# Performance work log

Hardware: AMD Instinct MI355X
Metric: run time of the kernel (lower is better)

Reference implementation:

```python
import jax, jax.numpy as jnp
import numpy as np

# Static routing config (must match init_kwargs)
E = 16          # num_experts
G = 4           # n_group
EPG = E // G    # experts per group
K = 4           # moe_router_topk
TOPK_GROUP = 2  # moe_topk_group
PER_GROUP_K = K // TOPK_GROUP


def setup_inputs() -> dict:
    key = jax.random.key(0)
    ks = jax.random.split(key, 9)
    B, T, C, H, HS = 2, 1024, 1024, 256, 2048
    std = 0.02
    return {
        'x': jax.random.normal(ks[0], (B, T, C), jnp.float32),
        'router_w': jax.random.normal(ks[1], (E, C), jnp.float32) * std,
        'correction_bias': jnp.zeros((E,), jnp.float32),
        'gate_w': jax.random.normal(ks[2], (E, C, H), jnp.float32) * std,
        'up_w': jax.random.normal(ks[3], (E, C, H), jnp.float32) * std,
        'down_w': jax.random.normal(ks[4], (E, H, C), jnp.float32) * std,
        'shared_gate_w': jax.random.normal(ks[5], (HS, C), jnp.float32) * std,
        'shared_up_w': jax.random.normal(ks[6], (HS, C), jnp.float32) * std,
        'shared_down_w': jax.random.normal(ks[7], (C, HS), jnp.float32) * std,
    }


def _route(xf, router_w, correction_bias):
    # Grouped sigmoid top-k routing (group_limited_greedy) with score correction bias.
    S = xf.shape[0]
    logits = xf @ router_w.T                       # [S, E]
    scores = jax.nn.sigmoid(logits)
    sb = scores + correction_bias                  # biased scores (selection only)
    # group score = sum of top (K // topk_group) biased scores within each group
    grp_top = jax.lax.top_k(sb.reshape(S, G, EPG), PER_GROUP_K)[0]
    group_scores = grp_top.sum(axis=-1)            # [S, G]
    _, group_idx = jax.lax.top_k(group_scores, TOPK_GROUP)
    group_mask = jnp.zeros((S, G), sb.dtype).at[jnp.arange(S)[:, None], group_idx].set(1.0)
    score_mask = jnp.broadcast_to(group_mask[:, :, None], (S, G, EPG)).reshape(S, E)
    masked = jnp.where(score_mask > 0, sb, -jnp.inf)
    _, topk_idx = jax.lax.top_k(masked, K)         # [S, K]
    # final weights come from UNBIASED sigmoid scores, renormalized over top-k
    w = jnp.take_along_axis(scores, topk_idx, axis=1)
    w = w / (w.sum(axis=-1, keepdims=True) + 1e-20)
    return topk_idx, w, scores


def reference(x, router_w, correction_bias, gate_w, up_w, down_w,
              shared_gate_w, shared_up_w, shared_down_w):
    B, T, C = x.shape
    S = B * T
    xf = x.reshape(S, C)
    # shared expert (always-on SwiGLU FFN)
    sg = xf @ shared_gate_w.T
    su = xf @ shared_up_w.T
    shared_out = (jax.nn.silu(sg) * su) @ shared_down_w.T          # [S, C]
    # routing
    topk_idx, w, _scores = _route(xf, router_w, correction_bias)
    combine = jnp.zeros((S, E), xf.dtype).at[jnp.arange(S)[:, None], topk_idx].add(w)  # [S, E]
    # routed experts: SwiGLU per expert (dense dispatch, combine weights fold the sparsity)
    g = jnp.einsum('sc,ech->esh', xf, gate_w)
    u = jnp.einsum('sc,ech->esh', xf, up_w)
    h = jax.nn.silu(g) * u                                         # [E, S, H]
    hw = h * combine.T[:, :, None]                                 # weight before down-proj
    routed = jnp.einsum('esh,ehc->sc', hw, down_w)                 # [S, C]
    return (shared_out + routed).reshape(B, T, C)
```

## Files before the change

### kernel.cpp

```cpp
#include <hip/hip_runtime.h>
#include <hip/hip_bf16.h>
#include <math.h>

#define S 2048
#define CDIM 1024
#define H 256
#define HS 2048
#define E 16
#define GNUM 4
#define EPG 4
#define TOPK 4
#define KSLICES 8

typedef __attribute__((ext_vector_type(8))) short bfrag_t;
typedef __attribute__((ext_vector_type(4))) float facc_t;
typedef __attribute__((ext_vector_type(4))) unsigned int u32x4;
typedef __attribute__((ext_vector_type(4))) unsigned short u16x4;

__device__ __forceinline__ float sigmoidf_(float v) { return 1.f / (1.f + __expf(-v)); }

__device__ __forceinline__ unsigned short f2bf(float f) {
    union { float f; unsigned u; } v; v.f = f;
    unsigned r = v.u + 0x7FFFu + ((v.u >> 16) & 1u);
    return (unsigned short)(r >> 16);
}
__device__ __forceinline__ float bf2f(unsigned short u) {
    union { unsigned u; float f; } v; v.u = ((unsigned)u) << 16; return v.f;
}
__device__ __forceinline__ unsigned long long pack4(float4 v) {
    return (unsigned long long)f2bf(v.x)
         | ((unsigned long long)f2bf(v.y) << 16)
         | ((unsigned long long)f2bf(v.z) << 32)
         | ((unsigned long long)f2bf(v.w) << 48);
}

__device__ __forceinline__ void stage16(const unsigned short* g, unsigned short* l, int lane) {
#if __has_builtin(__builtin_amdgcn_global_load_lds)
    __builtin_amdgcn_global_load_lds(
        (const __attribute__((address_space(1))) void*)g,
        (__attribute__((address_space(3))) void*)l, 16, 0, 0);
#else
    *(u32x4*)(l + lane * 8) = *(const u32x4*)g;
#endif
}

struct CastArgs {
    const float4* src[3];
    unsigned long long* dst[3];
};

#define LG_BLOCKS   ((S / 16) * KSLICES)
#define CAST_BLOCKS (3 * (HS * CDIM / 4 / 256))
#define TGU_BLOCKS  (2 * E * (CDIM / 64) * (H / 64))
#define TDN_BLOCKS  (E * (H / 64) * (CDIM / 64))

__global__ __launch_bounds__(256) void preproc_kernel(
    const float* __restrict__ x, const float* __restrict__ rw,
    float* __restrict__ lgpart, unsigned short* __restrict__ xb,
    CastArgs ca,
    const float* __restrict__ gate_w, unsigned short* __restrict__ gwT,
    const float* __restrict__ up_w,  unsigned short* __restrict__ uwT,
    const float* __restrict__ down_w, unsigned short* __restrict__ dwT)
{
    __shared__ __align__(16) float tbuf[64 * 65];
    const int tid = threadIdx.x;
    int id = blockIdx.x;

    if (id < LG_BLOCKS) {
        const int ks = id >> 7;
        const int s0 = (id & 127) * 16;
        const int t = tid & 15, e = tid >> 4;
        const float4* xp = (const float4*)(x + (size_t)(s0 + t) * CDIM + ks * (CDIM / KSLICES));
        const float4* wp = (const float4*)(rw + (size_t)e * CDIM + ks * (CDIM / KSLICES));
        float acc = 0.f;
#pragma unroll 8
        for (int c = 0; c < CDIM / KSLICES / 4; ++c) {
            float4 xv = xp[c], wv = wp[c];
            acc += xv.x * wv.x + xv.y * wv.y + xv.z * wv.z + xv.w * wv.w;
        }
        float4 v0 = xp[e * 2], v1 = xp[e * 2 + 1];
        unsigned long long* dst = (unsigned long long*)
            (xb + (size_t)(s0 + t) * CDIM + ks * (CDIM / KSLICES) + e * 8);
        dst[0] = pack4(v0);
        dst[1] = pack4(v1);
        lgpart[((size_t)ks * S + s0 + t) * E + e] = acc;
        return;
    }
    id -= LG_BLOCKS;

    if (id < CAST_BLOCKS) {
        const int buf = id >> 11;
        const int i = (id & 2047) * 256 + tid;
        ca.dst[buf][i] = pack4(ca.src[buf][i]);
        return;
    }
    id -= CAST_BLOCKS;

    const float* src; unsigned short* dst; int R, Cc, zz, c0, r0;
    if (id < TGU_BLOCKS) {
        const int bx = id & 3; const int by = (id >> 2) & 15; const int bz = id >> 6;
        R = CDIM; Cc = H;
        src = (bz < E) ? gate_w : up_w;
        dst = (bz < E) ? gwT : uwT;
        zz = (bz < E) ? bz : bz - E;
        c0 = bx * 64; r0 = by * 64;
    } else {
        id -= TGU_BLOCKS;
        const int bx = id & 15; const int by = (id >> 4) & 3; const int bz = id >> 6;
        R = H; Cc = CDIM;
        src = down_w; dst = dwT; zz = bz;
        c0 = bx * 64; r0 = by * 64;
    }
    const size_t mo = (size_t)zz * R * Cc;
    src += mo; dst += mo;
    const int tx = tid & 15, ty = tid >> 4;
#pragma unroll
    for (int i = 0; i < 4; ++i) {
        const int row = ty + 16 * i;
        float4 v = *(const float4*)&src[(size_t)(r0 + row) * Cc + c0 + tx * 4];
        float* p = &tbuf[row * 65 + tx * 4];
        p[0] = v.x; p[1] = v.y; p[2] = v.z; p[3] = v.w;
    }
    __syncthreads();
#pragma unroll
    for (int j = 0; j < 4; ++j) {
        const int c = ty + 16 * j;
        u16x4 o;
#pragma unroll
        for (int i = 0; i < 4; ++i)
            o[i] = f2bf(tbuf[(tx * 4 + i) * 65 + c]);
        *(u16x4*)&dst[(size_t)(c0 + c) * R + r0 + tx * 4] = o;
    }
}

__global__ __launch_bounds__(256) void route_kernel(
    const float* __restrict__ lgpart, const float* __restrict__ bias,
    int* __restrict__ counts, int* __restrict__ list, float* __restrict__ wlist)
{
    __shared__ int lcount[E];
    __shared__ int lbase[E];
    const int tid = threadIdx.x;
    const int s = blockIdx.x * 256 + tid;
    if (tid < E) lcount[tid] = 0;
    float lgv[E];
#pragma unroll
    for (int i = 0; i < E; ++i) lgv[i] = 0.f;
#pragma unroll
    for (int ks = 0; ks < KSLICES; ++ks) {
        const float4* p = (const float4*)(lgpart + ((size_t)ks * S + s) * E);
#pragma unroll
        for (int q = 0; q < 4; ++q) {
            float4 v = p[q];
            lgv[q * 4 + 0] += v.x; lgv[q * 4 + 1] += v.y;
            lgv[q * 4 + 2] += v.z; lgv[q * 4 + 3] += v.w;
        }
    }
    float sc[E], sb[E];
#pragma unroll
    for (int e2 = 0; e2 < E; ++e2) {
        sc[e2] = 1.f / (1.f + __expf(-lgv[e2]));
        sb[e2] = sc[e2] + bias[e2];
    }
    float gsc[GNUM];
#pragma unroll
    for (int g = 0; g < GNUM; ++g) {
        int b_ = g * EPG;
        int m1 = 0; float v1 = sb[b_];
#pragma unroll
        for (int j = 1; j < EPG; ++j) if (sb[b_ + j] > v1) { v1 = sb[b_ + j]; m1 = j; }
        float v2 = -1e30f;
#pragma unroll
        for (int j = 0; j < EPG; ++j) if (j != m1 && sb[b_ + j] > v2) v2 = sb[b_ + j];
        gsc[g] = v1 + v2;
    }
    int g1 = 0;
#pragma unroll
    for (int g = 1; g < GNUM; ++g) if (gsc[g] > gsc[g1]) g1 = g;
    int g2 = (g1 == 0) ? 1 : 0;
#pragma unroll
    for (int g = 0; g < GNUM; ++g) if (g != g1 && gsc[g] > gsc[g2]) g2 = g;
    bool allowed[E];
#pragma unroll
    for (int e2 = 0; e2 < E; ++e2) {
        int g = e2 >> 2;
        allowed[e2] = (g == g1) || (g == g2);
    }
    int idx[TOPK]; float wk[TOPK];
#pragma unroll
    for (int k = 0; k < TOPK; ++k) {
        int best = 0; float bv = -1e30f;
#pragma unroll
        for (int e2 = 0; e2 < E; ++e2)
            if (allowed[e2] && sb[e2] > bv) { bv = sb[e2]; best = e2; }
        allowed[best] = false;
        idx[k] = best;
        wk[k] = sc[best];
    }
    float inv = 1.f / (wk[0] + wk[1] + wk[2] + wk[3] + 1e-20f);
    __syncthreads();
    int lpos[TOPK];
#pragma unroll
    for (int k = 0; k < TOPK; ++k)
        lpos[k] = atomicAdd(&lcount[idx[k]], 1);
    __syncthreads();
    if (tid < E)
        lbase[tid] = atomicAdd(&counts[tid], lcount[tid]);
    __syncthreads();
#pragma unroll
    for (int k = 0; k < TOPK; ++k) {
        int ee = idx[k];
        int pos = lbase[ee] + lpos[k];
        list[ee * S + pos] = s | (k << 16);
        wlist[ee * S + pos] = wk[k] * inv;
    }
}


__global__ __launch_bounds__(256) void gemm_shared_gateup(
    const unsigned short* __restrict__ xb, const unsigned short* __restrict__ gb,
    const unsigned short* __restrict__ ub, unsigned short* __restrict__ shb)
{
    __shared__ __align__(16) unsigned short As[2 * 128 * 32];
    __shared__ __align__(16) unsigned short Bg[2 * 64 * 32];
    __shared__ __align__(16) unsigned short Bu[2 * 64 * 32];
    const int tid = threadIdx.x;
    const int lane = tid & 63, w = tid >> 6;
    const int l15 = lane & 15, q = lane >> 4;
    const int r0 = blockIdx.y * 128;
    const int c0 = blockIdx.x * 64;
    const int wr = (w >> 1) * 64, wc = (w & 1) * 32;
    const int Lrow = lane >> 2;
    const int gseg = (lane & 3) ^ ((lane >> 3) & 3);
    const unsigned short* gA1 = xb + (size_t)(r0 + w * 16 + Lrow) * CDIM + gseg * 8;
    const unsigned short* gA2 = gA1 + (size_t)64 * CDIM;
    const unsigned short* gG  = gb + (size_t)(c0 + w * 16 + Lrow) * CDIM + gseg * 8;
    const unsigned short* gU  = ub + (size_t)(c0 + w * 16 + Lrow) * CDIM + gseg * 8;
    unsigned short* lA1 = &As[(w * 16) * 32];
    unsigned short* lA2 = lA1 + 64 * 32;
    unsigned short* lG  = &Bg[(w * 16) * 32];
    unsigned short* lU  = &Bu[(w * 16) * 32];
    const int swq = (q ^ ((l15 >> 1) & 3)) * 8;
    facc_t accg[4][2], accu[4][2];
#pragma unroll
    for (int i = 0; i < 4; ++i)
#pragma unroll
        for (int j = 0; j < 2; ++j) { accg[i][j] = 0.f; accu[i][j] = 0.f; }
    for (int k0 = 0; k0 < CDIM; k0 += 64) {
        stage16(gA1 + k0,      lA1,             lane);
        stage16(gA1 + k0 + 32, lA1 + 128 * 32,  lane);
        stage16(gA2 + k0,      lA2,             lane);
        stage16(gA2 + k0 + 32, lA2 + 128 * 32,  lane);
        stage16(gG + k0,       lG,              lane);
        stage16(gG + k0 + 32,  lG + 64 * 32,    lane);
        stage16(gU + k0,       lU,              lane);
        stage16(gU + k0 + 32,  lU + 64 * 32,    lane);
        __syncthreads();
#pragma unroll
        for (int kk = 0; kk < 2; ++kk) {
            const unsigned short* Ah = &As[kk * 128 * 32];
            const unsigned short* Gh = &Bg[kk * 64 * 32];
            const unsigned short* Uh = &Bu[kk * 64 * 32];
            bfrag_t af[4], gf[2], uf[2];
#pragma unroll
            for (int i = 0; i < 4; ++i)
                af[i] = *(const bfrag_t*)&Ah[(wr + i * 16 + l15) * 32 + swq];
#pragma unroll
            for (int j = 0; j < 2; ++j) {
                gf[j] = *(const bfrag_t*)&Gh[(wc + j * 16 + l15) * 32 + swq];
                uf[j] = *(const bfrag_t*)&Uh[(wc + j * 16 + l15) * 32 + swq];
            }
#pragma unroll
            for (int i = 0; i < 4; ++i)
#pragma unroll
                for (int j = 0; j < 2; ++j) {
                    accg[i][j] = __builtin_amdgcn_mfma_f32_16x16x32_bf16(af[i], gf[j], accg[i][j], 0, 0, 0);
                    accu[i][j] = __builtin_amdgcn_mfma_f32_16x16x32_bf16(af[i], uf[j], accu[i][j], 0, 0, 0);
                }
        }
        __syncthreads();
    }
#pragma unroll
    for (int i = 0; i < 4; ++i)
#pragma unroll
        for (int j = 0; j < 2; ++j)
#pragma unroll
            for (int r = 0; r < 4; ++r) {
                int row = r0 + wr + i * 16 + q * 4 + r;
                int col = c0 + wc + j * 16 + l15;
                float g = accg[i][j][r], u = accu[i][j][r];
                shb[(size_t)row * HS + col] = f2bf(g * sigmoidf_(g) * u);
            }
}

__global__ __launch_bounds__(256) void gemm_shared_down(
    const unsigned short* __restrict__ shb, const unsigned short* __restrict__ db,
    const unsigned short* __restrict__ dbuf, float* __restrict__ out)
{
    __shared__ __align__(16) unsigned short As[2 * 64 * 32];
    __shared__ __align__(16) unsigned short Bs[2 * 64 * 32];
    const int tid = threadIdx.x;
    const int lane = tid & 63, w = tid >> 6;
    const int l15 = lane & 15, q = lane >> 4;
    const int r0 = blockIdx.y * 64;
    const int c0 = blockIdx.x * 64;
    const int wr = (w >> 1) * 32, wc = (w & 1) * 32;
    const int Lrow = lane >> 2;
    const int gseg = (lane & 3) ^ ((lane >> 3) & 3);
    const unsigned short* gA = shb + (size_t)(r0 + w * 16 + Lrow) * HS + gseg * 8;
    const unsigned short* gB = db + (size_t)(c0 + w * 16 + Lrow) * HS + gseg * 8;
    unsigned short* lA = &As[(w * 16) * 32];
    unsigned short* lB = &Bs[(w * 16) * 32];
    const int swq = (q ^ ((l15 >> 1) & 3)) * 8;
    facc_t acc[2][2];
#pragma unroll
    for (int i = 0; i < 2; ++i)
#pragma unroll
        for (int j = 0; j < 2; ++j) acc[i][j] = 0.f;
    for (int k0 = 0; k0 < HS; k0 += 64) {
        stage16(gA + k0,      lA,            lane);
        stage16(gA + k0 + 32, lA + 64 * 32,  lane);
        stage16(gB + k0,      lB,            lane);
        stage16(gB + k0 + 32, lB + 64 * 32,  lane);
        __syncthreads();
#pragma unroll
        for (int kk = 0; kk < 2; ++kk) {
            const unsigned short* Ah = &As[kk * 64 * 32];
            const unsigned short* Bh = &Bs[kk * 64 * 32];
            bfrag_t af[2], bf[2];
#pragma unroll
            for (int i = 0; i < 2; ++i) af[i] = *(const bfrag_t*)&Ah[(wr + i * 16 + l15) * 32 + swq];
#pragma unroll
            for (int j = 0; j < 2; ++j) bf[j] = *(const bfrag_t*)&Bh[(wc + j * 16 + l15) * 32 + swq];
#pragma unroll
            for (int i = 0; i < 2; ++i)
#pragma unroll
                for (int j = 0; j < 2; ++j)
                    acc[i][j] = __builtin_amdgcn_mfma_f32_16x16x32_bf16(af[i], bf[j], acc[i][j], 0, 0, 0);
        }
        __syncthreads();
    }
#pragma unroll
    for (int i = 0; i < 2; ++i)
#pragma unroll
        for (int j = 0; j < 2; ++j)
#pragma unroll
            for (int r = 0; r < 4; ++r) {
                int row = r0 + wr + i * 16 + q * 4 + r;
                int col = c0 + wc + j * 16 + l15;
                float v = acc[i][j][r];
                const unsigned short* dp = dbuf + ((size_t)row * TOPK) * CDIM + col;
#pragma unroll
                for (int k = 0; k < TOPK; ++k) v += bf2f(dp[(size_t)k * CDIM]);
                out[(size_t)row * CDIM + col] = v;
            }
}

__global__ __launch_bounds__(256) void gemm_routed_gateup(
    const unsigned short* __restrict__ xb, const unsigned short* __restrict__ gwT,
    const unsigned short* __restrict__ uwT, const int* __restrict__ counts,
    const int* __restrict__ list, const float* __restrict__ wlist,
    unsigned short* __restrict__ hbuf)
{
    const int e = blockIdx.x;
    const int n = counts[e];
    const int t0 = blockIdx.z * 64;
    if (t0 >= n) return;
    const int h0 = blockIdx.y * 64;
    __shared__ int toks[64];
    __shared__ int hrw[64];
    __shared__ float wv[64];
    __shared__ __align__(16) unsigned short As[2 * 64 * 32];
    __shared__ __align__(16) unsigned short Bg[2 * 64 * 32];
    __shared__ __align__(16) unsigned short Bu[2 * 64 * 32];
    const int tid = threadIdx.x;
    if (tid < 64) {
        int p = t0 + tid;
        if (p < n) {
            int pk = list[e * S + p];
            toks[tid] = pk & 0xFFFF;
            hrw[tid] = (pk & 0xFFFF) * TOPK + (pk >> 16);
            wv[tid] = wlist[e * S + p];
        } else { toks[tid] = 0; hrw[tid] = 0; wv[tid] = 0.f; }
    }
    __syncthreads();
    const int lane = tid & 63, w = tid >> 6;
    const int l15 = lane & 15, q = lane >> 4;
    const int wr = (w >> 1) * 32, wc = (w & 1) * 32;
    const int Lrow = lane >> 2;
    const int gseg = (lane & 3) ^ ((lane >> 3) & 3);
    const int tokA = toks[w * 16 + Lrow];
    const unsigned short* gA = xb + (size_t)tokA * CDIM + gseg * 8;
    const unsigned short* gG = gwT + ((size_t)e * H + h0 + w * 16 + Lrow) * CDIM + gseg * 8;
    const unsigned short* gU = uwT + ((size_t)e * H + h0 + w * 16 + Lrow) * CDIM + gseg * 8;
    unsigned short* lA = &As[(w * 16) * 32];
    unsigned short* lG = &Bg[(w * 16) * 32];
    unsigned short* lU = &Bu[(w * 16) * 32];
    const int swq = (q ^ ((l15 >> 1) & 3)) * 8;
    facc_t accg[2][2], accu[2][2];
#pragma unroll
    for (int i = 0; i < 2; ++i)
#pragma unroll
        for (int j = 0; j < 2; ++j) { accg[i][j] = 0.f; accu[i][j] = 0.f; }
    for (int k0 = 0; k0 < CDIM; k0 += 64) {
        stage16(gA + k0,      lA,            lane);
        stage16(gA + k0 + 32, lA + 64 * 32,  lane);
        stage16(gG + k0,      lG,            lane);
        stage16(gG + k0 + 32, lG + 64 * 32,  lane);
        stage16(gU + k0,      lU,            lane);
        stage16(gU + k0 + 32, lU + 64 * 32,  lane);
        __syncthreads();
#pragma unroll
        for (int kk = 0; kk < 2; ++kk) {
            const unsigned short* Ah = &As[kk * 64 * 32];
            const unsigned short* Gh = &Bg[kk * 64 * 32];
            const unsigned short* Uh = &Bu[kk * 64 * 32];
            bfrag_t af[2], gf[2], uf[2];
#pragma unroll
            for (int i = 0; i < 2; ++i) af[i] = *(const bfrag_t*)&Ah[(wr + i * 16 + l15) * 32 + swq];
#pragma unroll
            for (int j = 0; j < 2; ++j) {
                gf[j] = *(const bfrag_t*)&Gh[(wc + j * 16 + l15) * 32 + swq];
                uf[j] = *(const bfrag_t*)&Uh[(wc + j * 16 + l15) * 32 + swq];
            }
#pragma unroll
            for (int i = 0; i < 2; ++i)
#pragma unroll
                for (int j = 0; j < 2; ++j) {
                    accg[i][j] = __builtin_amdgcn_mfma_f32_16x16x32_bf16(af[i], gf[j], accg[i][j], 0, 0, 0);
                    accu[i][j] = __builtin_amdgcn_mfma_f32_16x16x32_bf16(af[i], uf[j], accu[i][j], 0, 0, 0);
                }
        }
        __syncthreads();
    }
#pragma unroll
    for (int i = 0; i < 2; ++i)
#pragma unroll
        for (int j = 0; j < 2; ++j)
#pragma unroll
            for (int r = 0; r < 4; ++r) {
                int li = wr + i * 16 + q * 4 + r;
                if (t0 + li < n) {
                    int col = h0 + wc + j * 16 + l15;
                    float g = accg[i][j][r], u = accu[i][j][r];
                    hbuf[(size_t)hrw[li] * H + col] = f2bf(wv[li] * g * sigmoidf_(g) * u);
                }
            }
}

__global__ __launch_bounds__(256) void gemm_routed_down(
    const unsigned short* __restrict__ hbuf, const unsigned short* __restrict__ dwT,
    const int* __restrict__ counts, const int* __restrict__ list,
    unsigned short* __restrict__ dbuf)
{
    const int e = blockIdx.x;
    const int n = counts[e];
    const int t0 = blockIdx.z * 64;
    if (t0 >= n) return;
    const int c0 = blockIdx.y * 64;
    __shared__ int hrw[64];
    __shared__ __align__(16) unsigned short As[2 * 64 * 32];
    __shared__ __align__(16) unsigned short Bs[2 * 64 * 32];
    const int tid = threadIdx.x;
    if (tid < 64) {
        int p = t0 + tid;
        int pk = (p < n) ? list[e * S + p] : 0;
        hrw[tid] = (pk & 0xFFFF) * TOPK + (pk >> 16);
    }
    __syncthreads();
    const int lane = tid & 63, w = tid >> 6;
    const int l15 = lane & 15, q = lane >> 4;
    const int wr = (w >> 1) * 32, wc = (w & 1) * 32;
    const int Lrow = lane >> 2;
    const int gseg = (lane & 3) ^ ((lane >> 3) & 3);
    const int arow = hrw[w * 16 + Lrow];
    const unsigned short* gA = hbuf + (size_t)arow * H + gseg * 8;
    const unsigned short* gB = dwT + ((size_t)e * CDIM + c0 + w * 16 + Lrow) * H + gseg * 8;
    unsigned short* lA = &As[(w * 16) * 32];
    unsigned short* lB = &Bs[(w * 16) * 32];
    const int swq = (q ^ ((l15 >> 1) & 3)) * 8;
    facc_t acc[2][2];
#pragma unroll
    for (int i = 0; i < 2; ++i)
#pragma unroll
        for (int j = 0; j < 2; ++j) acc[i][j] = 0.f;
    for (int k0 = 0; k0 < H; k0 += 64) {
        stage16(gA + k0,      lA,            lane);
        stage16(gA + k0 + 32, lA + 64 * 32,  lane);
        stage16(gB + k0,      lB,            lane);
        stage16(gB + k0 + 32, lB + 64 * 32,  lane);
        __syncthreads();
#pragma unroll
        for (int kk = 0; kk < 2; ++kk) {
            const unsigned short* Ah = &As[kk * 64 * 32];
            const unsigned short* Bh = &Bs[kk * 64 * 32];
            bfrag_t af[2], bf[2];
#pragma unroll
            for (int i = 0; i < 2; ++i) af[i] = *(const bfrag_t*)&Ah[(wr + i * 16 + l15) * 32 + swq];
#pragma unroll
            for (int j = 0; j < 2; ++j) bf[j] = *(const bfrag_t*)&Bh[(wc + j * 16 + l15) * 32 + swq];
#pragma unroll
            for (int i = 0; i < 2; ++i)
#pragma unroll
                for (int j = 0; j < 2; ++j)
                    acc[i][j] = __builtin_amdgcn_mfma_f32_16x16x32_bf16(af[i], bf[j], acc[i][j], 0, 0, 0);
        }
        __syncthreads();
    }
#pragma unroll
    for (int i = 0; i < 2; ++i)
#pragma unroll
        for (int j = 0; j < 2; ++j)
#pragma unroll
            for (int r = 0; r < 4; ++r) {
                int li = wr + i * 16 + q * 4 + r;
                if (t0 + li < n) {
                    int col = c0 + wc + j * 16 + l15;
                    dbuf[(size_t)hrw[li] * CDIM + col] = f2bf(acc[i][j][r]);
                }
            }
}

extern "C" void kernel_launch(void* const* d_in, const int* in_sizes, int n_in,
                              void* d_out, int out_size, void* d_ws, size_t ws_size,
                              hipStream_t stream)
{
    const float* x        = (const float*)d_in[0];
    const float* router_w = (const float*)d_in[1];
    const float* bias     = (const float*)d_in[2];
    const float* gate_w   = (const float*)d_in[3];
    const float* up_w     = (const float*)d_in[4];
    const float* down_w   = (const float*)d_in[5];
    const float* sgw      = (const float*)d_in[6];
    const float* suw      = (const float*)d_in[7];
    const float* sdw      = (const float*)d_in[8];
    float* out = (float*)d_out;

    char* ws = (char*)d_ws;
    size_t off = 0;
    int* counts = (int*)(ws + off);            off += 256;
    int* list   = (int*)(ws + off);            off += (size_t)E * S * 4;
    float* wlist = (float*)(ws + off);         off += (size_t)E * S * 4;
    unsigned short* xb  = (unsigned short*)(ws + off); off += (size_t)S * CDIM * 2;
    unsigned short* sgb = (unsigned short*)(ws + off); off += (size_t)HS * CDIM * 2;
    unsigned short* sub = (unsigned short*)(ws + off); off += (size_t)HS * CDIM * 2;
    unsigned short* sdb = (unsigned short*)(ws + off); off += (size_t)CDIM * HS * 2;
    unsigned short* gwT = (unsigned short*)(ws + off); off += (size_t)E * H * CDIM * 2;
    unsigned short* uwT = (unsigned short*)(ws + off); off += (size_t)E * H * CDIM * 2;
    unsigned short* dwT = (unsigned short*)(ws + off); off += (size_t)E * CDIM * H * 2;
    unsigned short* shb = (unsigned short*)(ws + off); off += (size_t)S * HS * 2;
    unsigned short* hbuf = (unsigned short*)(ws + off); off += (size_t)S * TOPK * H * 2;
    unsigned short* dbuf = (unsigned short*)(ws + off); off += (size_t)S * TOPK * CDIM * 2;
    float* lgpart = (float*)dbuf;

    hipMemsetAsync(counts, 0, E * sizeof(int), stream);

    CastArgs ca;
    ca.src[0] = (const float4*)sgw; ca.dst[0] = (unsigned long long*)sgb;
    ca.src[1] = (const float4*)suw; ca.dst[1] = (unsigned long long*)sub;
    ca.src[2] = (const float4*)sdw; ca.dst[2] = (unsigned long long*)sdb;

    preproc_kernel<<<LG_BLOCKS + CAST_BLOCKS + TGU_BLOCKS + TDN_BLOCKS, 256, 0, stream>>>(
        x, router_w, lgpart, xb, ca, gate_w, gwT, up_w, uwT, down_w, dwT);

    route_kernel<<<S / 256, 256, 0, stream>>>(lgpart, bias, counts, list, wlist);

    gemm_shared_gateup<<<dim3(HS / 64, S / 128), 256, 0, stream>>>(xb, sgb, sub, shb);
    gemm_routed_gateup<<<dim3(E, H / 64, S / 64), 256, 0, stream>>>(xb, gwT, uwT, counts, list, wlist, hbuf);
    gemm_routed_down<<<dim3(E, CDIM / 64, S / 64), 256, 0, stream>>>(hbuf, dwT, counts, list, dbuf);
    gemm_shared_down<<<dim3(CDIM / 64, S / 64), 256, 0, stream>>>(shb, sdb, dbuf, out);
}
```

Before: 226.7 us.

## Fuse shared and routed gate-up GEMMs into one launch, enlarge M tiles

Merges the shared-expert and routed-expert gate/up GEMMs into a single kernel. A flat block index selects which branch each block runs, so both workloads share one launch and can fill the GPU together. The routed gate-up, routed down and shared down kernels also move from 64-row to 128-row tiles, giving each warp 4x2 MFMA tiles for more operand reuse per LDS load. The cost is more registers and LDS per block and fewer blocks overall, which may lower occupancy. Routed experts with few tokens also waste more padding rows per tile.

```diff
diff --git a/kernel.cpp b/kernel.cpp
--- a/kernel.cpp
+++ b/kernel.cpp
@@ -215,36 +215,74 @@
     }
 }
 
-
-__global__ __launch_bounds__(256) void gemm_shared_gateup(
+#define K4_BLOCKS ((HS / 64) * (S / 128))
+#define K6_BLOCKS (E * (H / 64) * (S / 128))
+
+__global__ __launch_bounds__(256) void gemm_gateup_fused(
     const unsigned short* __restrict__ xb, const unsigned short* __restrict__ gb,
-    const unsigned short* __restrict__ ub, unsigned short* __restrict__ shb)
+    const unsigned short* __restrict__ ub, unsigned short* __restrict__ shb,
+    const unsigned short* __restrict__ gwT, const unsigned short* __restrict__ uwT,
+    const int* __restrict__ counts, const int* __restrict__ list,
+    const float* __restrict__ wlist, unsigned short* __restrict__ hbuf)
 {
     __shared__ __align__(16) unsigned short As[2 * 128 * 32];
     __shared__ __align__(16) unsigned short Bg[2 * 64 * 32];
     __shared__ __align__(16) unsigned short Bu[2 * 64 * 32];
+    __shared__ int toks[128];
+    __shared__ int hrw[128];
+    __shared__ float wv[128];
+
     const int tid = threadIdx.x;
     const int lane = tid & 63, w = tid >> 6;
     const int l15 = lane & 15, q = lane >> 4;
-    const int r0 = blockIdx.y * 128;
-    const int c0 = blockIdx.x * 64;
     const int wr = (w >> 1) * 64, wc = (w & 1) * 32;
     const int Lrow = lane >> 2;
     const int gseg = (lane & 3) ^ ((lane >> 3) & 3);
-    const unsigned short* gA1 = xb + (size_t)(r0 + w * 16 + Lrow) * CDIM + gseg * 8;
-    const unsigned short* gA2 = gA1 + (size_t)64 * CDIM;
-    const unsigned short* gG  = gb + (size_t)(c0 + w * 16 + Lrow) * CDIM + gseg * 8;
-    const unsigned short* gU  = ub + (size_t)(c0 + w * 16 + Lrow) * CDIM + gseg * 8;
+    const int swq = (q ^ ((l15 >> 1) & 3)) * 8;
+
+    const bool isK4 = (int)blockIdx.x < K4_BLOCKS;
+    const unsigned short *gA1, *gA2, *gG, *gU;
+    int n = 0, t0 = 0, r0 = 0, cb = 0, e = 0;
+    if (isK4) {
+        cb = ((int)blockIdx.x & 31) * 64;
+        r0 = ((int)blockIdx.x >> 5) * 128;
+        gA1 = xb + (size_t)(r0 + w * 16 + Lrow) * CDIM + gseg * 8;
+        gA2 = gA1 + (size_t)64 * CDIM;
+        gG  = gb + (size_t)(cb + w * 16 + Lrow) * CDIM + gseg * 8;
+        gU  = ub + (size_t)(cb + w * 16 + Lrow) * CDIM + gseg * 8;
+    } else {
+        const int id2 = (int)blockIdx.x - K4_BLOCKS;
+        e  = id2 >> 6;
+        cb = ((id2 >> 4) & 3) * 64;
+        t0 = (id2 & 15) * 128;
+        n  = counts[e];
+        if (t0 >= n) return;
+        if (tid < 128) {
+            int p = t0 + tid;
+            if (p < n) {
+                int pk = list[e * S + p];
+                toks[tid] = pk & 0xFFFF;
+                hrw[tid] = (pk & 0xFFFF) * TOPK + (pk >> 16);
+                wv[tid] = wlist[e * S + p];
+            } else { toks[tid] = 0; hrw[tid] = 0; wv[tid] = 0.f; }
+        }
+        __syncthreads();
+        gA1 = xb + (size_t)toks[w * 16 + Lrow] * CDIM + gseg * 8;
+        gA2 = xb + (size_t)toks[64 + w * 16 + Lrow] * CDIM + gseg * 8;
+        gG = gwT + ((size_t)e * H + cb + w * 16 + Lrow) * CDIM + gseg * 8;
+        gU = uwT + ((size_t)e * H + cb + w * 16 + Lrow) * CDIM + gseg * 8;
+    }
     unsigned short* lA1 = &As[(w * 16) * 32];
     unsigned short* lA2 = lA1 + 64 * 32;
     unsigned short* lG  = &Bg[(w * 16) * 32];
     unsigned short* lU  = &Bu[(w * 16) * 32];
-    const int swq = (q ^ ((l15 >> 1) & 3)) * 8;
+
     facc_t accg[4][2], accu[4][2];
 #pragma unroll
     for (int i = 0; i < 4; ++i)
 #pragma unroll
         for (int j = 0; j < 2; ++j) { accg[i][j] = 0.f; accu[i][j] = 0.f; }
+
     for (int k0 = 0; k0 < CDIM; k0 += 64) {
         stage16(gA1 + k0,      lA1,             lane);
         stage16(gA1 + k0 + 32, lA1 + 128 * 32,  lane);
@@ -279,172 +317,34 @@
         }
         __syncthreads();
     }
-#pragma unroll
-    for (int i = 0; i < 4; ++i)
-#pragma unroll
-        for (int j = 0; j < 2; ++j)
-#pragma unroll
-            for (int r = 0; r < 4; ++r) {
-                int row = r0 + wr + i * 16 + q * 4 + r;
-                int col = c0 + wc + j * 16 + l15;
-                float g = accg[i][j][r], u = accu[i][j][r];
-                shb[(size_t)row * HS + col] = f2bf(g * sigmoidf_(g) * u);
-            }
-}
-
-__global__ __launch_bounds__(256) void gemm_shared_down(
-    const unsigned short* __restrict__ shb, const unsigned short* __restrict__ db,
-    const unsigned short* __restrict__ dbuf, float* __restrict__ out)
-{
-    __shared__ __align__(16) unsigned short As[2 * 64 * 32];
-    __shared__ __align__(16) unsigned short Bs[2 * 64 * 32];
-    const int tid = threadIdx.x;
-    const int lane = tid & 63, w = tid >> 6;
-    const int l15 = lane & 15, q = lane >> 4;
-    const int r0 = blockIdx.y * 64;
-    const int c0 = blockIdx.x * 64;
-    const int wr = (w >> 1) * 32, wc = (w & 1) * 32;
-    const int Lrow = lane >> 2;
-    const int gseg = (lane & 3) ^ ((lane >> 3) & 3);
-    const unsigned short* gA = shb + (size_t)(r0 + w * 16 + Lrow) * HS + gseg * 8;
-    const unsigned short* gB = db + (size_t)(c0 + w * 16 + Lrow) * HS + gseg * 8;
-    unsigned short* lA = &As[(w * 16) * 32];
-    unsigned short* lB = &Bs[(w * 16) * 32];
-    const int swq = (q ^ ((l15 >> 1) & 3)) * 8;
-    facc_t acc[2][2];
-#pragma unroll
-    for (int i = 0; i < 2; ++i)
-#pragma unroll
-        for (int j = 0; j < 2; ++j) acc[i][j] = 0.f;
-    for (int k0 = 0; k0 < HS; k0 += 64) {
-        stage16(gA + k0,      lA,            lane);
-        stage16(gA + k0 + 32, lA + 64 * 32,  lane);
-        stage16(gB + k0,      lB,            lane);
-        stage16(gB + k0 + 32, lB + 64 * 32,  lane);
-        __syncthreads();
-#pragma unroll
-        for (int kk = 0; kk < 2; ++kk) {
-            const unsigned short* Ah = &As[kk * 64 * 32];
-            const unsigned short* Bh = &Bs[kk * 64 * 32];
-            bfrag_t af[2], bf[2];
-#pragma unroll
-            for (int i = 0; i < 2; ++i) af[i] = *(const bfrag_t*)&Ah[(wr + i * 16 + l15) * 32 + swq];
-#pragma unroll
-            for (int j = 0; j < 2; ++j) bf[j] = *(const bfrag_t*)&Bh[(wc + j * 16 + l15) * 32 + swq];
-#pragma unroll
-            for (int i = 0; i < 2; ++i)
-#pragma unroll
-                for (int j = 0; j < 2; ++j)
-                    acc[i][j] = __builtin_amdgcn_mfma_f32_16x16x32_bf16(af[i], bf[j], acc[i][j], 0, 0, 0);
-        }
-        __syncthreads();
-    }
-#pragma unroll
-    for (int i = 0; i < 2; ++i)
-#pragma unroll
-        for (int j = 0; j < 2; ++j)
-#pragma unroll
-            for (int r = 0; r < 4; ++r) {
-                int row = r0 + wr + i * 16 + q * 4 + r;
-                int col = c0 + wc + j * 16 + l15;
-                float v = acc[i][j][r];
-                const unsigned short* dp = dbuf + ((size_t)row * TOPK) * CDIM + col;
-#pragma unroll
-                for (int k = 0; k < TOPK; ++k) v += bf2f(dp[(size_t)k * CDIM]);
-                out[(size_t)row * CDIM + col] = v;
-            }
-}
-
-__global__ __launch_bounds__(256) void gemm_routed_gateup(
-    const unsigned short* __restrict__ xb, const unsigned short* __restrict__ gwT,
-    const unsigned short* __restrict__ uwT, const int* __restrict__ counts,
-    const int* __restrict__ list, const float* __restrict__ wlist,
-    unsigned short* __restrict__ hbuf)
-{
-    const int e = blockIdx.x;
-    const int n = counts[e];
-    const int t0 = blockIdx.z * 64;
-    if (t0 >= n) return;
-    const int h0 = blockIdx.y * 64;
-    __shared__ int toks[64];
-    __shared__ int hrw[64];
-    __shared__ float wv[64];
-    __shared__ __align__(16) unsigned short As[2 * 64 * 32];
-    __shared__ __align__(16) unsigned short Bg[2 * 64 * 32];
-    __shared__ __align__(16) unsigned short Bu[2 * 64 * 32];
-    const int tid = threadIdx.x;
-    if (tid < 64) {
-        int p = t0 + tid;
-        if (p < n) {
-            int pk = list[e * S + p];
-            toks[tid] = pk & 0xFFFF;
-            hrw[tid] = (pk & 0xFFFF) * TOPK + (pk >> 16);
-            wv[tid] = wlist[e * S + p];
-        } else { toks[tid] = 0; hrw[tid] = 0; wv[tid] = 0.f; }
-    }
-    __syncthreads();
-    const int lane = tid & 63, w = tid >> 6;
-    const int l15 = lane & 15, q = lane >> 4;
-    const int wr = (w >> 1) * 32, wc = (w & 1) * 32;
-    const int Lrow = lane >> 2;
-    const int gseg = (lane & 3) ^ ((lane >> 3) & 3);
-    const int tokA = toks[w * 16 + Lrow];
-    const unsigned short* gA = xb + (size_t)tokA * CDIM + gseg * 8;
-    const unsigned short* gG = gwT + ((size_t)e * H + h0 + w * 16 + Lrow) * CDIM + gseg * 8;
-    const unsigned short* gU = uwT + ((size_t)e * H + h0 + w * 16 + Lrow) * CDIM + gseg * 8;
-    unsigned short* lA = &As[(w * 16) * 32];
-    unsigned short* lG = &Bg[(w * 16) * 32];
-    unsigned short* lU = &Bu[(w * 16) * 32];
-    const int swq = (q ^ ((l15 >> 1) & 3)) * 8;
-    facc_t accg[2][2], accu[2][2];
-#pragma unroll
-    for (int i = 0; i < 2; ++i)
-#pragma unroll
-        for (int j = 0; j < 2; ++j) { accg[i][j] = 0.f; accu[i][j] = 0.f; }
-    for (int k0 = 0; k0 < CDIM; k0 += 64) {
-        stage16(gA + k0,      lA,            lane);
-        stage16(gA + k0 + 32, lA + 64 * 32,  lane);
-        stage16(gG + k0,      lG,            lane);
-        stage16(gG + k0 + 32, lG + 64 * 32,  lane);
-        stage16(gU + k0,      lU,            lane);
-        stage16(gU + k0 + 32, lU + 64 * 32,  lane);
-        __syncthreads();
-#pragma unroll
-        for (int kk = 0; kk < 2; ++kk) {
-            const unsigned short* Ah = &As[kk * 64 * 32];
-            const unsigned short* Gh = &Bg[kk * 64 * 32];
-            const unsigned short* Uh = &Bu[kk * 64 * 32];
-            bfrag_t af[2], gf[2], uf[2];
-#pragma unroll
-            for (int i = 0; i < 2; ++i) af[i] = *(const bfrag_t*)&Ah[(wr + i * 16 + l15) * 32 + swq];
-#pragma unroll
-            for (int j = 0; j < 2; ++j) {
-                gf[j] = *(const bfrag_t*)&Gh[(wc + j * 16 + l15) * 32 + swq];
-                uf[j] = *(const bfrag_t*)&Uh[(wc + j * 16 + l15) * 32 + swq];
-            }
-#pragma unroll
-            for (int i = 0; i < 2; ++i)
-#pragma unroll
-                for (int j = 0; j < 2; ++j) {
-                    accg[i][j] = __builtin_amdgcn_mfma_f32_16x16x32_bf16(af[i], gf[j], accg[i][j], 0, 0, 0);
-                    accu[i][j] = __builtin_amdgcn_mfma_f32_16x16x32_bf16(af[i], uf[j], accu[i][j], 0, 0, 0);
+
+    if (isK4) {
+#pragma unroll
+        for (int i = 0; i < 4; ++i)
+#pragma unroll
+            for (int j = 0; j < 2; ++j)
+#pragma unroll
+                for (int r = 0; r < 4; ++r) {
+                    int row = r0 + wr + i * 16 + q * 4 + r;
+                    int col = cb + wc + j * 16 + l15;
+                    float g = accg[i][j][r], u = accu[i][j][r];
+                    shb[(size_t)row * HS + col] = f2bf(g * sigmoidf_(g) * u);
                 }
-        }
-        __syncthreads();
-    }
-#pragma unroll
-    for (int i = 0; i < 2; ++i)
-#pragma unroll
-        for (int j = 0; j < 2; ++j)
-#pragma unroll
-            for (int r = 0; r < 4; ++r) {
-                int li = wr + i * 16 + q * 4 + r;
-                if (t0 + li < n) {
-                    int col = h0 + wc + j * 16 + l15;
-                    float g = accg[i][j][r], u = accu[i][j][r];
-                    hbuf[(size_t)hrw[li] * H + col] = f2bf(wv[li] * g * sigmoidf_(g) * u);
+    } else {
+#pragma unroll
+        for (int i = 0; i < 4; ++i)
+#pragma unroll
+            for (int j = 0; j < 2; ++j)
+#pragma unroll
+                for (int r = 0; r < 4; ++r) {
+                    int li = wr + i * 16 + q * 4 + r;
+                    if (t0 + li < n) {
+                        int col = cb + wc + j * 16 + l15;
+                        float g = accg[i][j][r], u = accu[i][j][r];
+                        hbuf[(size_t)hrw[li] * H + col] = f2bf(wv[li] * g * sigmoidf_(g) * u);
+                    }
                 }
-            }
+    }
 }
 
 __global__ __launch_bounds__(256) void gemm_routed_down(
@@ -454,14 +354,14 @@
 {
     const int e = blockIdx.x;
     const int n = counts[e];
-    const int t0 = blockIdx.z * 64;
+    const int t0 = blockIdx.z * 128;
     if (t0 >= n) return;
     const int c0 = blockIdx.y * 64;
-    __shared__ int hrw[64];
-    __shared__ __align__(16) unsigned short As[2 * 64 * 32];
+    __shared__ int hrw[128];
+    __shared__ __align__(16) unsigned short As[2 * 128 * 32];
     __shared__ __align__(16) unsigned short Bs[2 * 64 * 32];
     const int tid = threadIdx.x;
-    if (tid < 64) {
+    if (tid < 128) {
         int p = t0 + tid;
         int pk = (p < n) ? list[e * S + p] : 0;
         hrw[tid] = (pk & 0xFFFF) * TOPK + (pk >> 16);
@@ -469,37 +369,40 @@
     __syncthreads();
     const int lane = tid & 63, w = tid >> 6;
     const int l15 = lane & 15, q = lane >> 4;
-    const int wr = (w >> 1) * 32, wc = (w & 1) * 32;
+    const int wr = (w >> 1) * 64, wc = (w & 1) * 32;
     const int Lrow = lane >> 2;
     const int gseg = (lane & 3) ^ ((lane >> 3) & 3);
-    const int arow = hrw[w * 16 + Lrow];
-    const unsigned short* gA = hbuf + (size_t)arow * H + gseg * 8;
+    const unsigned short* gA1 = hbuf + (size_t)hrw[w * 16 + Lrow] * H + gseg * 8;
+    const unsigned short* gA2 = hbuf + (size_t)hrw[64 + w * 16 + Lrow] * H + gseg * 8;
     const unsigned short* gB = dwT + ((size_t)e * CDIM + c0 + w * 16 + Lrow) * H + gseg * 8;
-    unsigned short* lA = &As[(w * 16) * 32];
+    unsigned short* lA1 = &As[(w * 16) * 32];
+    unsigned short* lA2 = lA1 + 64 * 32;
     unsigned short* lB = &Bs[(w * 16) * 32];
     const int swq = (q ^ ((l15 >> 1) & 3)) * 8;
-    facc_t acc[2][2];
-#pragma unroll
-    for (int i = 0; i < 2; ++i)
+    facc_t acc[4][2];
+#pragma unroll
+    for (int i = 0; i < 4; ++i)
 #pragma unroll
         for (int j = 0; j < 2; ++j) acc[i][j] = 0.f;
     for (int k0 = 0; k0 < H; k0 += 64) {
-        stage16(gA + k0,      lA,            lane);
-        stage16(gA + k0 + 32, lA + 64 * 32,  lane);
-        stage16(gB + k0,      lB,            lane);
-        stage16(gB + k0 + 32, lB + 64 * 32,  lane);
+        stage16(gA1 + k0,      lA1,            lane);
+        stage16(gA1 + k0 + 32, lA1 + 128 * 32, lane);
+        stage16(gA2 + k0,      lA2,            lane);
+        stage16(gA2 + k0 + 32, lA2 + 128 * 32, lane);
+        stage16(gB + k0,       lB,             lane);
+        stage16(gB + k0 + 32,  lB + 64 * 32,   lane);
         __syncthreads();
 #pragma unroll
         for (int kk = 0; kk < 2; ++kk) {
-            const unsigned short* Ah = &As[kk * 64 * 32];
+            const unsigned short* Ah = &As[kk * 128 * 32];
             const unsigned short* Bh = &Bs[kk * 64 * 32];
-            bfrag_t af[2], bf[2];
-#pragma unroll
-            for (int i = 0; i < 2; ++i) af[i] = *(const bfrag_t*)&Ah[(wr + i * 16 + l15) * 32 + swq];
+            bfrag_t af[4], bf[2];
+#pragma unroll
+            for (int i = 0; i < 4; ++i) af[i] = *(const bfrag_t*)&Ah[(wr + i * 16 + l15) * 32 + swq];
 #pragma unroll
             for (int j = 0; j < 2; ++j) bf[j] = *(const bfrag_t*)&Bh[(wc + j * 16 + l15) * 32 + swq];
 #pragma unroll
-            for (int i = 0; i < 2; ++i)
+            for (int i = 0; i < 4; ++i)
 #pragma unroll
                 for (int j = 0; j < 2; ++j)
                     acc[i][j] = __builtin_amdgcn_mfma_f32_16x16x32_bf16(af[i], bf[j], acc[i][j], 0, 0, 0);
@@ -507,7 +410,7 @@
         __syncthreads();
     }
 #pragma unroll
-    for (int i = 0; i < 2; ++i)
+    for (int i = 0; i < 4; ++i)
 #pragma unroll
         for (int j = 0; j < 2; ++j)
 #pragma unroll
@@ -517,6 +420,73 @@
                     int col = c0 + wc + j * 16 + l15;
                     dbuf[(size_t)hrw[li] * CDIM + col] = f2bf(acc[i][j][r]);
                 }
+            }
+}
+
+__global__ __launch_bounds__(256) void gemm_shared_down(
+    const unsigned short* __restrict__ shb, const unsigned short* __restrict__ db,
+    const unsigned short* __restrict__ dbuf, float* __restrict__ out)
+{
+    __shared__ __align__(16) unsigned short As[2 * 128 * 32];
+    __shared__ __align__(16) unsigned short Bs[2 * 64 * 32];
+    const int tid = threadIdx.x;
+    const int lane = tid & 63, w = tid >> 6;
+    const int l15 = lane & 15, q = lane >> 4;
+    const int r0 = blockIdx.y * 128;
+    const int c0 = blockIdx.x * 64;
+    const int wr = (w >> 1) * 64, wc = (w & 1) * 32;
+    const int Lrow = lane >> 2;
+    const int gseg = (lane & 3) ^ ((lane >> 3) & 3);
+    const unsigned short* gA1 = shb + (size_t)(r0 + w * 16 + Lrow) * HS + gseg * 8;
+    const unsigned short* gA2 = gA1 + (size_t)64 * HS;
+    const unsigned short* gB = db + (size_t)(c0 + w * 16 + Lrow) * HS + gseg * 8;
+    unsigned short* lA1 = &As[(w * 16) * 32];
+    unsigned short* lA2 = lA1 + 64 * 32;
+    unsigned short* lB = &Bs[(w * 16) * 32];
+    const int swq = (q ^ ((l15 >> 1) & 3)) * 8;
+    facc_t acc[4][2];
+#pragma unroll
+    for (int i = 0; i < 4; ++i)
+#pragma unroll
+        for (int j = 0; j < 2; ++j) acc[i][j] = 0.f;
+    for (int k0 = 0; k0 < HS; k0 += 64) {
+        stage16(gA1 + k0,      lA1,            lane);
+        stage16(gA1 + k0 + 32, lA1 + 128 * 32, lane);
+        stage16(gA2 + k0,      lA2,            lane);
+        stage16(gA2 + k0 + 32, lA2 + 128 * 32, lane);
+        stage16(gB + k0,       lB,             lane);
+        stage16(gB + k0 + 32,  lB + 64 * 32,   lane);
+        __syncthreads();
+#pragma unroll
+        for (int kk = 0; kk < 2; ++kk) {
+            const unsigned short* Ah = &As[kk * 128 * 32];
+            const unsigned short* Bh = &Bs[kk * 64 * 32];
+            bfrag_t af[4], bf[2];
+#pragma unroll
+            for (int i = 0; i < 4; ++i) af[i] = *(const bfrag_t*)&Ah[(wr + i * 16 + l15) * 32 + swq];
+#pragma unroll
+            for (int j = 0; j < 2; ++j) bf[j] = *(const bfrag_t*)&Bh[(wc + j * 16 + l15) * 32 + swq];
+#pragma unroll
+            for (int i = 0; i < 4; ++i)
+#pragma unroll
+                for (int j = 0; j < 2; ++j)
+                    acc[i][j] = __builtin_amdgcn_mfma_f32_16x16x32_bf16(af[i], bf[j], acc[i][j], 0, 0, 0);
+        }
+        __syncthreads();
+    }
+#pragma unroll
+    for (int i = 0; i < 4; ++i)
+#pragma unroll
+        for (int j = 0; j < 2; ++j)
+#pragma unroll
+            for (int r = 0; r < 4; ++r) {
+                int row = r0 + wr + i * 16 + q * 4 + r;
+                int col = c0 + wc + j * 16 + l15;
+                float v = acc[i][j][r];
+                const unsigned short* dp = dbuf + ((size_t)row * TOPK) * CDIM + col;
+#pragma unroll
+                for (int k = 0; k < TOPK; ++k) v += bf2f(dp[(size_t)k * CDIM]);
+                out[(size_t)row * CDIM + col] = v;
             }
 }
 
@@ -564,8 +534,9 @@
 
     route_kernel<<<S / 256, 256, 0, stream>>>(lgpart, bias, counts, list, wlist);
 
-    gemm_shared_gateup<<<dim3(HS / 64, S / 128), 256, 0, stream>>>(xb, sgb, sub, shb);
-    gemm_routed_gateup<<<dim3(E, H / 64, S / 64), 256, 0, stream>>>(xb, gwT, uwT, counts, list, wlist, hbuf);
-    gemm_routed_down<<<dim3(E, CDIM / 64, S / 64), 256, 0, stream>>>(hbuf, dwT, counts, list, dbuf);
-    gemm_shared_down<<<dim3(CDIM / 64, S / 64), 256, 0, stream>>>(shb, sdb, dbuf, out);
-}
+    gemm_gateup_fused<<<K4_BLOCKS + K6_BLOCKS, 256, 0, stream>>>(
+        xb, sgb, sub, shb, gwT, uwT, counts, list, wlist, hbuf);
+
+    gemm_routed_down<<<dim3(E, CDIM / 64, S / 128), 256, 0, stream>>>(hbuf, dwT, counts, list, dbuf);
+    gemm_shared_down<<<dim3(CDIM / 64, S / 128), 256, 0, stream>>>(shb, sdb, dbuf, out);
+}
```

After: 258.5 us. 1.14x slower.
